# Performance work log

Measured on AMD Instinct MI355X. Metric: run time of the kernel, lower is better.

## Reference

```python
import jax, jax.numpy as jnp
import numpy as np

N = 200000   # nodes
E = 6400000  # edges (avg degree 32)
T = 6        # member feature dim
M = 10       # fingerprint dim
L = 4        # R + 1 layers
GIN = 14     # group_level_input
GLO = 10     # group_level_output


def setup_inputs() -> dict:
    key = jax.random.key(0)
    ks = jax.random.split(key, 10)
    return {
        "x_member": jax.random.normal(ks[0], (N, T), dtype=jnp.float32),
        "x_group": jax.random.normal(ks[1], (1, GIN), dtype=jnp.float32),
        "src": jax.random.randint(ks[2], (E,), 0, N, dtype=jnp.int32),
        "dst": jax.random.randint(ks[3], (E,), 0, N, dtype=jnp.int32),
        "H": jax.random.normal(ks[4], (L, T, M), dtype=jnp.float32),
        "W": jax.random.normal(ks[5], (L,), dtype=jnp.float32),
        "gW": jax.random.normal(ks[6], (GLO, GIN), dtype=jnp.float32) * 0.1,
        "gb": jax.random.normal(ks[7], (GLO,), dtype=jnp.float32),
        "mW": jax.random.normal(ks[8], (3, M + GLO), dtype=jnp.float32) * 0.1,
        "mb": jax.random.normal(ks[9], (3,), dtype=jnp.float32),
    }


def reference(x_member, x_group, src, dst, H, W, gW, gb, mW, mb):
    n = x_member.shape[0]
    # message passing: neighbor feature sum per destination node  [N, T]
    neigh = jax.ops.segment_sum(x_member[src], dst, num_segments=n)
    v1 = x_member + neigh  # r[a] + sum of neighbor r's; r is layer-invariant
    # all R+1 layers at once: [L, N, M]
    v2 = jax.nn.sigmoid(jnp.einsum("nt,ltm->lnm", v1, H))
    fl = jax.nn.softmax(v2 * W[:, None, None], axis=-1)
    # f starts at zeros and accumulates softmax over every node and layer -> [1, M]
    f = jnp.sum(fl, axis=(0, 1))[None, :]
    # group-level perceptron
    g = jax.nn.sigmoid(x_group @ gW.T + gb)  # [1, GLO]
    merged = jnp.concatenate([f, g], axis=1)  # [1, M+GLO]
    return jax.nn.softmax(merged @ mW.T + mb, axis=-1)  # [1, 3]
```

## Files before the change

### kernel.cpp

```cpp
#include <hip/hip_runtime.h>
#include <hip/hip_fp16.h>
#include <math.h>

#define TDIM 6
#define MDIM 10
#define LDIM 4
#define GIND 14
#define GLOD 10

#define BINSHIFT 8
#define BINSZ 256
#define MAXBINS 1024

#define SC2_BLOCKS 512
#define SC2_THREADS 512
#define SC2_KQ 7
#define OVF_ENT 16384
#define META2 2048

#define SC_BLOCK 512
#define SC_EPT 32
#define SC_EPB (SC_BLOCK * SC_EPT)
#define AC_BLOCK 512
#define AC_CAP 10240
#define AC_EPT 20

__global__ void zero32_k(unsigned* __restrict__ p, int n) {
    int i = blockIdx.x * blockDim.x + threadIdx.x;
    if (i < n) p[i] = 0u;
}


__global__ __launch_bounds__(SC2_THREADS) void scat2_k(
        const float* __restrict__ xm, int N, uint4* __restrict__ xh,
        const int* __restrict__ src, const int* __restrict__ dst, int E, int NQ, int QPB,
        unsigned* __restrict__ gcount, unsigned* __restrict__ ebuf, int C, int nbins,
        uint2* __restrict__ ovf, unsigned* __restrict__ ocur) {
    __shared__ unsigned lcount[MAXBINS];
    __shared__ unsigned lbase[MAXBINS];
    int tid = threadIdx.x;
    for (int i = tid; i < MAXBINS; i += SC2_THREADS) lcount[i] = 0u;

    int gid = blockIdx.x * SC2_THREADS + tid;
    int gstride = gridDim.x * SC2_THREADS;
    for (int n = gid; n < N; n += gstride) {
        const float2* r = (const float2*)(xm + (size_t)n * TDIM);
        float2 a = r[0], b = r[1], c = r[2];
        __half2 h0 = __floats2half2_rn(a.x, a.y);
        __half2 h1 = __floats2half2_rn(b.x, b.y);
        __half2 h2 = __floats2half2_rn(c.x, c.y);
        uint4 o;
        o.x = *(unsigned*)&h0; o.y = *(unsigned*)&h1; o.z = *(unsigned*)&h2; o.w = 0u;
        xh[n] = o;
    }
    if (blockIdx.x == 0) {
        for (int e = NQ * 4 + tid; e < E; e += SC2_THREADS) {
            unsigned oc = atomicAdd(ocur, 1u);
            if (oc < OVF_ENT) ovf[oc] = make_uint2((unsigned)src[e], (unsigned)dst[e]);
        }
    }
    __syncthreads();

    int qb = blockIdx.x * QPB;
    int qend = qb + QPB; if (qend > NQ) qend = NQ;
    const int4* s4p = (const int4*)src;
    const int4* d4p = (const int4*)dst;

    unsigned pk[SC2_KQ * 4];
    unsigned wr[SC2_KQ * 4];

#pragma unroll
    for (int i = 0; i < SC2_KQ; i++) {
        int q = qb + tid + i * SC2_THREADS;
        if (q < qend) {
            int4 sv = s4p[q];
            int4 dv = d4p[q];
            {
                unsigned du = (unsigned)dv.x, b = du >> BINSHIFT;
                pk[i*4+0] = ((du & (BINSZ-1)) << 18) | (unsigned)sv.x;
                wr[i*4+0] = (b << 18) | atomicAdd(&lcount[b], 1u);
            }
            {
                unsigned du = (unsigned)dv.y, b = du >> BINSHIFT;
                pk[i*4+1] = ((du & (BINSZ-1)) << 18) | (unsigned)sv.y;
                wr[i*4+1] = (b << 18) | atomicAdd(&lcount[b], 1u);
            }
            {
                unsigned du = (unsigned)dv.z, b = du >> BINSHIFT;
                pk[i*4+2] = ((du & (BINSZ-1)) << 18) | (unsigned)sv.z;
                wr[i*4+2] = (b << 18) | atomicAdd(&lcount[b], 1u);
            }
            {
                unsigned du = (unsigned)dv.w, b = du >> BINSHIFT;
                pk[i*4+3] = ((du & (BINSZ-1)) << 18) | (unsigned)sv.w;
                wr[i*4+3] = (b << 18) | atomicAdd(&lcount[b], 1u);
            }
        } else {
            pk[i*4+0] = 0xFFFFFFFFu; pk[i*4+1] = 0xFFFFFFFFu;
            pk[i*4+2] = 0xFFFFFFFFu; pk[i*4+3] = 0xFFFFFFFFu;
        }
    }
    __syncthreads();

    for (int i = tid; i < nbins; i += SC2_THREADS) {
        unsigned c = lcount[i];
        if (c) lbase[i] = atomicAdd(&gcount[i], c);
    }
    __syncthreads();

#pragma unroll
    for (int k = 0; k < SC2_KQ * 4; k++) {
        unsigned p = pk[k];
        if (p != 0xFFFFFFFFu) {
            unsigned b = wr[k] >> 18;
            unsigned pos = lbase[b] + (wr[k] & 0x3FFFFu);
            if (pos < (unsigned)C) {
                ebuf[b * (unsigned)C + pos] = p;
            } else {
                unsigned oc = atomicAdd(ocur, 1u);
                if (oc < OVF_ENT) {
                    unsigned s = p & 0x3FFFFu;
                    unsigned d = (b << BINSHIFT) | (p >> 18);
                    ovf[oc] = make_uint2(s, d);
                }
            }
        }
    }
}

__global__ __launch_bounds__(AC_BLOCK) void accum2_k(
        const float* __restrict__ xm, const uint4* __restrict__ xh,
        const unsigned* __restrict__ ebuf, const unsigned* __restrict__ gcount, int C,
        const unsigned* __restrict__ ocur, const uint2* __restrict__ ovf,
        const float* __restrict__ H, const float* __restrict__ W,
        float* __restrict__ facc, int N) {
    __shared__ unsigned srt[AC_CAP];
    __shared__ unsigned cnt[BINSZ];
    __shared__ unsigned tmp[BINSZ];
    __shared__ unsigned cstart[BINSZ];
    __shared__ unsigned ovl[256];
    __shared__ unsigned ovn;
    __shared__ float sH[LDIM * TDIM * MDIM];
    __shared__ float sW[LDIM];
    __shared__ float sred[AC_BLOCK / 64][MDIM];
    int tid = threadIdx.x;
    int bin = blockIdx.x;
    for (int i = tid; i < LDIM * TDIM * MDIM; i += AC_BLOCK) sH[i] = H[i];
    if (tid < LDIM) sW[tid] = W[tid];
    if (tid < BINSZ) cnt[tid] = 0u;
    if (tid == 0) ovn = 0u;
    __syncthreads();

    unsigned gc = gcount[bin];
    unsigned m = gc < (unsigned)C ? gc : (unsigned)C;
    unsigned e0 = (unsigned)bin * (unsigned)C;
    int nbase = bin << BINSHIFT;

    unsigned ed_[AC_EPT];
    unsigned rk_[AC_EPT];
#pragma unroll
    for (int k = 0; k < AC_EPT; k++) {
        unsigned i = (unsigned)tid + (unsigned)k * AC_BLOCK;
        if (i < m) {
            unsigned v = ebuf[e0 + i];
            ed_[k] = v;
            rk_[k] = atomicAdd(&cnt[v >> 18], 1u);
        }
    }
    {
        unsigned novf = *ocur;
        if (novf > OVF_ENT) novf = OVF_ENT;
        for (unsigned i = tid; i < novf; i += AC_BLOCK) {
            uint2 e = ovf[i];
            if ((e.y >> BINSHIFT) == (unsigned)bin) {
                unsigned u = atomicAdd(&ovn, 1u);
                if (u < 256u) ovl[u] = ((e.y & (BINSZ-1)) << 18) | e.x;
            }
        }
    }
    __syncthreads();

    if (tid < BINSZ) tmp[tid] = cnt[tid];
    __syncthreads();
    for (int off = 1; off < BINSZ; off <<= 1) {
        unsigned v = 0;
        if (tid < BINSZ) { v = tmp[tid]; if (tid >= off) v += tmp[tid - off]; }
        __syncthreads();
        if (tid < BINSZ) tmp[tid] = v;
        __syncthreads();
    }
    if (tid < BINSZ) cstart[tid] = tmp[tid] - cnt[tid];
    __syncthreads();

#pragma unroll
    for (int k = 0; k < AC_EPT; k++) {
        unsigned i = (unsigned)tid + (unsigned)k * AC_BLOCK;
        if (i < m) {
            unsigned v = ed_[k];
            srt[cstart[v >> 18] + rk_[k]] = v & 0x3FFFFu;
        }
    }
    __syncthreads();

    float fs[MDIM];
#pragma unroll
    for (int mm = 0; mm < MDIM; mm++) fs[mm] = 0.f;

    int n = nbase + tid;
    if (tid < BINSZ && n < N) {
        float s0 = 0.f, s1 = 0.f, s2 = 0.f, s3 = 0.f, s4 = 0.f, s5 = 0.f;
        unsigned c = cnt[tid];
        unsigned b0 = cstart[tid];
        unsigned j = 0;
        for (; j + 2 <= c; j += 2) {
            unsigned sa = srt[b0 + j], sb = srt[b0 + j + 1];
            uint4 ra = xh[sa];
            uint4 rb = xh[sb];
            float2 a0 = __half22float2(*(__half2*)&ra.x);
            float2 a1 = __half22float2(*(__half2*)&ra.y);
            float2 a2 = __half22float2(*(__half2*)&ra.z);
            float2 c0 = __half22float2(*(__half2*)&rb.x);
            float2 c1 = __half22float2(*(__half2*)&rb.y);
            float2 c2 = __half22float2(*(__half2*)&rb.z);
            s0 += a0.x + c0.x; s1 += a0.y + c0.y;
            s2 += a1.x + c1.x; s3 += a1.y + c1.y;
            s4 += a2.x + c2.x; s5 += a2.y + c2.y;
        }
        if (j < c) {
            uint4 ra = xh[srt[b0 + j]];
            float2 a0 = __half22float2(*(__half2*)&ra.x);
            float2 a1 = __half22float2(*(__half2*)&ra.y);
            float2 a2 = __half22float2(*(__half2*)&ra.z);
            s0 += a0.x; s1 += a0.y; s2 += a1.x; s3 += a1.y; s4 += a2.x; s5 += a2.y;
        }
        unsigned no = ovn < 256u ? ovn : 256u;
        for (unsigned q = 0; q < no; q++) {
            unsigned o = ovl[q];
            if ((int)(o >> 18) == tid) {
                uint4 ra = xh[o & 0x3FFFFu];
                float2 a0 = __half22float2(*(__half2*)&ra.x);
                float2 a1 = __half22float2(*(__half2*)&ra.y);
                float2 a2 = __half22float2(*(__half2*)&ra.z);
                s0 += a0.x; s1 += a0.y; s2 += a1.x; s3 += a1.y; s4 += a2.x; s5 += a2.y;
            }
        }

        float v[TDIM];
        const float2* xr = (const float2*)(xm + (size_t)n * TDIM);
        float2 x0 = xr[0], x1 = xr[1], x2 = xr[2];
        v[0] = x0.x + s0; v[1] = x0.y + s1;
        v[2] = x1.x + s2; v[3] = x1.y + s3;
        v[4] = x2.x + s4; v[5] = x2.y + s5;

#pragma unroll
        for (int l = 0; l < LDIM; l++) {
            float z[MDIM];
#pragma unroll
            for (int mm = 0; mm < MDIM; mm++) {
                float a2 = 0.f;
#pragma unroll
                for (int t = 0; t < TDIM; t++) a2 += v[t] * sH[(l * TDIM + t) * MDIM + mm];
                z[mm] = a2;
            }
            float wl = sW[l];
            float mx = -1e30f;
#pragma unroll
            for (int mm = 0; mm < MDIM; mm++) {
                float sg = wl / (1.f + __expf(-z[mm]));
                z[mm] = sg;
                mx = fmaxf(mx, sg);
            }
            float se = 0.f;
#pragma unroll
            for (int mm = 0; mm < MDIM; mm++) {
                float e = __expf(z[mm] - mx);
                z[mm] = e;
                se += e;
            }
            float inv = 1.f / se;
#pragma unroll
            for (int mm = 0; mm < MDIM; mm++) fs[mm] += z[mm] * inv;
        }
    }

#pragma unroll
    for (int mm = 0; mm < MDIM; mm++) {
        float v = fs[mm];
#pragma unroll
        for (int off = 32; off > 0; off >>= 1) v += __shfl_down(v, off, 64);
        fs[mm] = v;
    }
    int wave = tid >> 6, lane = tid & 63;
    if (lane == 0) {
#pragma unroll
        for (int mm = 0; mm < MDIM; mm++) sred[wave][mm] = fs[mm];
    }
    __syncthreads();
    if (tid < MDIM) {
        float s = 0.f;
#pragma unroll
        for (int w = 0; w < AC_BLOCK / 64; w++) s += sred[w][tid];
        atomicAdd(facc + tid, s);
    }
}


__global__ __launch_bounds__(256) void prep_k(const float* __restrict__ xm, int N,
                                              uint4* __restrict__ xh,
                                              const int* __restrict__ dst, int E,
                                              unsigned* __restrict__ hist, int nbins) {
    __shared__ unsigned lh[MAXBINS];
    for (int i = threadIdx.x; i < MAXBINS; i += blockDim.x) lh[i] = 0u;
    __syncthreads();
    int gid = blockIdx.x * blockDim.x + threadIdx.x;
    int gstride = gridDim.x * blockDim.x;
    for (int n = gid; n < N; n += gstride) {
        const float2* r = (const float2*)(xm + (size_t)n * TDIM);
        float2 a = r[0], b = r[1], c = r[2];
        __half2 h0 = __floats2half2_rn(a.x, a.y);
        __half2 h1 = __floats2half2_rn(b.x, b.y);
        __half2 h2 = __floats2half2_rn(c.x, c.y);
        uint4 o;
        o.x = *(unsigned*)&h0; o.y = *(unsigned*)&h1; o.z = *(unsigned*)&h2; o.w = 0u;
        xh[n] = o;
    }
    int e4 = E >> 2;
    const int4* d4p = (const int4*)dst;
    for (int i = gid; i < e4; i += gstride) {
        int4 d = d4p[i];
        atomicAdd(&lh[((unsigned)d.x) >> BINSHIFT], 1u);
        atomicAdd(&lh[((unsigned)d.y) >> BINSHIFT], 1u);
        atomicAdd(&lh[((unsigned)d.z) >> BINSHIFT], 1u);
        atomicAdd(&lh[((unsigned)d.w) >> BINSHIFT], 1u);
    }
    for (int e = (e4 << 2) + gid; e < E; e += gstride)
        atomicAdd(&lh[((unsigned)dst[e]) >> BINSHIFT], 1u);
    __syncthreads();
    for (int i = threadIdx.x; i < nbins; i += blockDim.x)
        if (lh[i]) atomicAdd(&hist[i], lh[i]);
}

__global__ __launch_bounds__(MAXBINS) void scan_k(const unsigned* __restrict__ hist,
                                                  unsigned* __restrict__ offsets,
                                                  unsigned* __restrict__ gfill, int nbins) {
    __shared__ unsigned buf[2][MAXBINS];
    int t = threadIdx.x;
    buf[0][t] = (t < nbins) ? hist[t] : 0u;
    __syncthreads();
    int cur = 0;
    for (int off = 1; off < MAXBINS; off <<= 1) {
        unsigned v = buf[cur][t];
        if (t >= off) v += buf[cur][t - off];
        buf[cur ^ 1][t] = v;
        __syncthreads();
        cur ^= 1;
    }
    if (t < nbins) {
        unsigned ex = t ? buf[cur][t - 1] : 0u;
        offsets[t] = ex;
        gfill[t] = ex;
    }
    if (t == 0) offsets[nbins] = buf[cur][nbins - 1];
}

__global__ __launch_bounds__(SC_BLOCK) void scatter_k(const int* __restrict__ src,
                                                      const int* __restrict__ dst, int E,
                                                      unsigned* __restrict__ gfill,
                                                      unsigned* __restrict__ ebuf, int nbins) {
    __shared__ unsigned lcount[MAXBINS];
    __shared__ unsigned lbase[MAXBINS];
    for (int i = threadIdx.x; i < MAXBINS; i += SC_BLOCK) lcount[i] = 0u;
    __syncthreads();
    int base = blockIdx.x * SC_EPB + threadIdx.x * SC_EPT;
    int s[SC_EPT], d[SC_EPT];
    unsigned rk[SC_EPT];
#pragma unroll
    for (int q = 0; q < SC_EPT / 4; q++) {
        int e = base + q * 4;
        if (e + 3 < E) {
            int4 s4 = *(const int4*)(src + e);
            int4 d4 = *(const int4*)(dst + e);
            s[q*4+0] = s4.x; s[q*4+1] = s4.y; s[q*4+2] = s4.z; s[q*4+3] = s4.w;
            d[q*4+0] = d4.x; d[q*4+1] = d4.y; d[q*4+2] = d4.z; d[q*4+3] = d4.w;
        } else {
#pragma unroll
            for (int k = 0; k < 4; k++) {
                int ee = e + k;
                s[q*4+k] = (ee < E) ? src[ee] : -1;
                d[q*4+k] = (ee < E) ? dst[ee] : 0;
            }
        }
    }
#pragma unroll
    for (int k = 0; k < SC_EPT; k++)
        if (s[k] >= 0) rk[k] = atomicAdd(&lcount[((unsigned)d[k]) >> BINSHIFT], 1u);
    __syncthreads();
    for (int i = threadIdx.x; i < nbins; i += SC_BLOCK) {
        unsigned c = lcount[i];
        if (c) lbase[i] = atomicAdd(&gfill[i], c);
    }
    __syncthreads();
#pragma unroll
    for (int k = 0; k < SC_EPT; k++) {
        if (s[k] >= 0) {
            unsigned du = (unsigned)d[k];
            unsigned b = du >> BINSHIFT;
            unsigned pack = ((du & (BINSZ - 1)) << 18) | (unsigned)s[k];
            ebuf[lbase[b] + rk[k]] = pack;
        }
    }
}

__global__ __launch_bounds__(AC_BLOCK) void accum_node_k(
        const float* __restrict__ xm, const uint4* __restrict__ xh,
        const unsigned* __restrict__ ebuf, const unsigned* __restrict__ offsets,
        const float* __restrict__ H, const float* __restrict__ W,
        float* __restrict__ facc, int N) {
    __shared__ unsigned srt[AC_CAP];
    __shared__ unsigned cnt[BINSZ];
    __shared__ unsigned tmp[BINSZ];
    __shared__ unsigned cstart[BINSZ];
    __shared__ float sH[LDIM * TDIM * MDIM];
    __shared__ float sW[LDIM];
    __shared__ float sred[AC_BLOCK / 64][MDIM];
    int tid = threadIdx.x;
    int bin = blockIdx.x;
    for (int i = tid; i < LDIM * TDIM * MDIM; i += AC_BLOCK) sH[i] = H[i];
    if (tid < LDIM) sW[tid] = W[tid];
    if (tid < BINSZ) cnt[tid] = 0u;
    __syncthreads();

    unsigned e0 = offsets[bin], e1 = offsets[bin + 1];
    unsigned total = e1 - e0;
    unsigned m = total < AC_CAP ? total : AC_CAP;
    int nbase = bin << BINSHIFT;

    unsigned ed_[AC_EPT];
    unsigned rk_[AC_EPT];
#pragma unroll
    for (int k = 0; k < AC_EPT; k++) {
        unsigned idx = e0 + (unsigned)tid + (unsigned)k * AC_BLOCK;
        if (idx < e0 + m) {
            unsigned v = ebuf[idx];
            ed_[k] = v;
            rk_[k] = atomicAdd(&cnt[v >> 18], 1u);
        }
    }
    __syncthreads();

    if (tid < BINSZ) tmp[tid] = cnt[tid];
    __syncthreads();
    for (int off = 1; off < BINSZ; off <<= 1) {
        unsigned v = 0;
        if (tid < BINSZ) { v = tmp[tid]; if (tid >= off) v += tmp[tid - off]; }
        __syncthreads();
        if (tid < BINSZ) tmp[tid] = v;
        __syncthreads();
    }
    if (tid < BINSZ) cstart[tid] = tmp[tid] - cnt[tid];
    __syncthreads();

#pragma unroll
    for (int k = 0; k < AC_EPT; k++) {
        unsigned idx = e0 + (unsigned)tid + (unsigned)k * AC_BLOCK;
        if (idx < e0 + m) {
            unsigned v = ed_[k];
            srt[cstart[v >> 18] + rk_[k]] = v & 0x3FFFFu;
        }
    }
    __syncthreads();

    float fs[MDIM];
#pragma unroll
    for (int mm = 0; mm < MDIM; mm++) fs[mm] = 0.f;

    int n = nbase + tid;
    if (tid < BINSZ && n < N) {
        float s0 = 0.f, s1 = 0.f, s2 = 0.f, s3 = 0.f, s4 = 0.f, s5 = 0.f;
        unsigned c = cnt[tid];
        unsigned b0 = cstart[tid];
        unsigned j = 0;
        for (; j + 2 <= c; j += 2) {
            unsigned sa = srt[b0 + j], sb = srt[b0 + j + 1];
            uint4 ra = xh[sa];
            uint4 rb = xh[sb];
            float2 a0 = __half22float2(*(__half2*)&ra.x);
            float2 a1 = __half22float2(*(__half2*)&ra.y);
            float2 a2 = __half22float2(*(__half2*)&ra.z);
            float2 c0 = __half22float2(*(__half2*)&rb.x);
            float2 c1 = __half22float2(*(__half2*)&rb.y);
            float2 c2 = __half22float2(*(__half2*)&rb.z);
            s0 += a0.x + c0.x; s1 += a0.y + c0.y;
            s2 += a1.x + c1.x; s3 += a1.y + c1.y;
            s4 += a2.x + c2.x; s5 += a2.y + c2.y;
        }
        if (j < c) {
            uint4 ra = xh[srt[b0 + j]];
            float2 a0 = __half22float2(*(__half2*)&ra.x);
            float2 a1 = __half22float2(*(__half2*)&ra.y);
            float2 a2 = __half22float2(*(__half2*)&ra.z);
            s0 += a0.x; s1 += a0.y; s2 += a1.x; s3 += a1.y; s4 += a2.x; s5 += a2.y;
        }
        for (unsigned idx = e0 + m; idx < e1; idx++) {
            unsigned v = ebuf[idx];
            if ((int)(v >> 18) == tid) {
                uint4 ra = xh[v & 0x3FFFFu];
                float2 a0 = __half22float2(*(__half2*)&ra.x);
                float2 a1 = __half22float2(*(__half2*)&ra.y);
                float2 a2 = __half22float2(*(__half2*)&ra.z);
                s0 += a0.x; s1 += a0.y; s2 += a1.x; s3 += a1.y; s4 += a2.x; s5 += a2.y;
            }
        }

        float v[TDIM];
        const float2* xr = (const float2*)(xm + (size_t)n * TDIM);
        float2 x0 = xr[0], x1 = xr[1], x2 = xr[2];
        v[0] = x0.x + s0; v[1] = x0.y + s1;
        v[2] = x1.x + s2; v[3] = x1.y + s3;
        v[4] = x2.x + s4; v[5] = x2.y + s5;

#pragma unroll
        for (int l = 0; l < LDIM; l++) {
            float z[MDIM];
#pragma unroll
            for (int mm = 0; mm < MDIM; mm++) {
                float a2 = 0.f;
#pragma unroll
                for (int t = 0; t < TDIM; t++) a2 += v[t] * sH[(l * TDIM + t) * MDIM + mm];
                z[mm] = a2;
            }
            float wl = sW[l];
            float mx = -1e30f;
#pragma unroll
            for (int mm = 0; mm < MDIM; mm++) {
                float sg = wl / (1.f + __expf(-z[mm]));
                z[mm] = sg;
                mx = fmaxf(mx, sg);
            }
            float se = 0.f;
#pragma unroll
            for (int mm = 0; mm < MDIM; mm++) {
                float e = __expf(z[mm] - mx);
                z[mm] = e;
                se += e;
            }
            float inv = 1.f / se;
#pragma unroll
            for (int mm = 0; mm < MDIM; mm++) fs[mm] += z[mm] * inv;
        }
    }

#pragma unroll
    for (int mm = 0; mm < MDIM; mm++) {
        float v = fs[mm];
#pragma unroll
        for (int off = 32; off > 0; off >>= 1) v += __shfl_down(v, off, 64);
        fs[mm] = v;
    }
    int wave = tid >> 6, lane = tid & 63;
    if (lane == 0) {
#pragma unroll
        for (int mm = 0; mm < MDIM; mm++) sred[wave][mm] = fs[mm];
    }
    __syncthreads();
    if (tid < MDIM) {
        float s = 0.f;
#pragma unroll
        for (int w = 0; w < AC_BLOCK / 64; w++) s += sred[w][tid];
        atomicAdd(facc + tid, s);
    }
}

__global__ void finalize_k(const float* __restrict__ facc,
                           const float* __restrict__ xg,
                           const float* __restrict__ gW,
                           const float* __restrict__ gb,
                           const float* __restrict__ mW,
                           const float* __restrict__ mb,
                           float* __restrict__ out) {
    if (threadIdx.x == 0 && blockIdx.x == 0) {
        float merged[MDIM + GLOD];
#pragma unroll
        for (int m = 0; m < MDIM; m++) merged[m] = facc[m];
        for (int j = 0; j < GLOD; j++) {
            float a = gb[j];
            for (int i = 0; i < GIND; i++) a += xg[i] * gW[j * GIND + i];
            merged[MDIM + j] = 1.f / (1.f + __expf(-a));
        }
        float lg[3];
        float mx = -1e30f;
        for (int k = 0; k < 3; k++) {
            float a = mb[k];
            for (int j = 0; j < MDIM + GLOD; j++) a += merged[j] * mW[k * (MDIM + GLOD) + j];
            lg[k] = a;
            mx = fmaxf(mx, a);
        }
        float se = 0.f;
        for (int k = 0; k < 3; k++) { lg[k] = __expf(lg[k] - mx); se += lg[k]; }
        float inv = 1.f / se;
        for (int k = 0; k < 3; k++) out[k] = lg[k] * inv;
    }
}

__global__ void fb_zero_k(float* __restrict__ ws, int n) {
    int i = blockIdx.x * blockDim.x + threadIdx.x;
    if (i < n) ws[i] = 0.f;
}

__global__ void fb_edge_scatter_k(const float* __restrict__ xm,
                                  const int* __restrict__ src,
                                  const int* __restrict__ dst,
                                  float* __restrict__ neigh, int E) {
    int e = blockIdx.x * blockDim.x + threadIdx.x;
    if (e >= E) return;
    int s = src[e], d = dst[e];
    const float2* r = (const float2*)(xm + (size_t)s * TDIM);
    float2 a = r[0], b = r[1], c = r[2];
    float* o = neigh + (size_t)d * TDIM;
    atomicAdd(o + 0, a.x); atomicAdd(o + 1, a.y);
    atomicAdd(o + 2, b.x); atomicAdd(o + 3, b.y);
    atomicAdd(o + 4, c.x); atomicAdd(o + 5, c.y);
}

__global__ __launch_bounds__(256) void fb_node_k(
        const float* __restrict__ xm, const float* __restrict__ neigh,
        const float* __restrict__ H, const float* __restrict__ W,
        float* __restrict__ facc, int N) {
    __shared__ float sH[LDIM * TDIM * MDIM];
    __shared__ float sW[LDIM];
    __shared__ float sred[4][MDIM];
    int tid = threadIdx.x;
    for (int i = tid; i < LDIM * TDIM * MDIM; i += blockDim.x) sH[i] = H[i];
    if (tid < LDIM) sW[tid] = W[tid];
    __syncthreads();
    float fs[MDIM];
#pragma unroll
    for (int m = 0; m < MDIM; m++) fs[m] = 0.f;
    for (int n = blockIdx.x * blockDim.x + tid; n < N; n += gridDim.x * blockDim.x) {
        float v[TDIM];
        const float2* xr = (const float2*)(xm + (size_t)n * TDIM);
        const float2* nr = (const float2*)(neigh + (size_t)n * TDIM);
#pragma unroll
        for (int t2 = 0; t2 < 3; t2++) {
            float2 a = xr[t2], b = nr[t2];
            v[2 * t2 + 0] = a.x + b.x;
            v[2 * t2 + 1] = a.y + b.y;
        }
#pragma unroll
        for (int l = 0; l < LDIM; l++) {
            float z[MDIM];
#pragma unroll
            for (int m = 0; m < MDIM; m++) {
                float a2 = 0.f;
#pragma unroll
                for (int t = 0; t < TDIM; t++) a2 += v[t] * sH[(l * TDIM + t) * MDIM + m];
                z[m] = a2;
            }
            float wl = sW[l], mx = -1e30f;
#pragma unroll
            for (int m = 0; m < MDIM; m++) { float sg = wl / (1.f + __expf(-z[m])); z[m] = sg; mx = fmaxf(mx, sg); }
            float se = 0.f;
#pragma unroll
            for (int m = 0; m < MDIM; m++) { float e = __expf(z[m] - mx); z[m] = e; se += e; }
            float inv = 1.f / se;
#pragma unroll
            for (int m = 0; m < MDIM; m++) fs[m] += z[m] * inv;
        }
    }
#pragma unroll
    for (int m = 0; m < MDIM; m++) {
        float v = fs[m];
#pragma unroll
        for (int off = 32; off > 0; off >>= 1) v += __shfl_down(v, off, 64);
        fs[m] = v;
    }
    int wave = tid >> 6, lane = tid & 63;
    if (lane == 0) {
#pragma unroll
        for (int m = 0; m < MDIM; m++) sred[wave][m] = fs[m];
    }
    __syncthreads();
    if (tid < MDIM) {
        float s = sred[0][tid] + sred[1][tid] + sred[2][tid] + sred[3][tid];
        atomicAdd(facc + tid, s);
    }
}

extern "C" void kernel_launch(void* const* d_in, const int* in_sizes, int n_in,
                              void* d_out, int out_size, void* d_ws, size_t ws_size,
                              hipStream_t stream) {
    const float* xm  = (const float*)d_in[0];
    const float* xg  = (const float*)d_in[1];
    const int*   src = (const int*)d_in[2];
    const int*   dst = (const int*)d_in[3];
    const float* H   = (const float*)d_in[4];
    const float* W   = (const float*)d_in[5];
    const float* gW  = (const float*)d_in[6];
    const float* gb  = (const float*)d_in[7];
    const float* mW  = (const float*)d_in[8];
    const float* mb  = (const float*)d_in[9];
    float* out = (float*)d_out;

    int N = in_sizes[0] / TDIM;
    int E = in_sizes[2];
    int nbins = (N + BINSZ - 1) >> BINSHIFT;
    size_t ws_words = ws_size / 4;
    size_t xh_words = (size_t)N * 4;

    long fixed = (long)(xh_words + META2 + (size_t)OVF_ENT * 2);
    long avail = (long)ws_words - fixed;
    long C = avail > 0 ? (avail / nbins) & ~3L : 0;
    if (C > AC_CAP) C = AC_CAP;
    double mu = (double)E / nbins;
    long Cmin = (long)(mu + 4.0 * sqrt(mu) + 32.0);
    int NQ = E >> 2;
    int QPB = (NQ + SC2_BLOCKS - 1) / SC2_BLOCKS;
    bool ok1 = (C >= Cmin) && nbins <= MAXBINS && N <= (1 << 18) &&
               QPB <= SC2_KQ * SC2_THREADS;

    size_t meta_words2 = MAXBINS + (MAXBINS + 1) + MAXBINS + 16;
    size_t need2 = (xh_words + (size_t)E + meta_words2) * 4;
    bool ok2 = ws_size >= need2 && nbins <= MAXBINS && N <= (1 << 18);

    if (ok1) {
        uint4*    xh     = (uint4*)d_ws;
        unsigned* ebuf   = (unsigned*)d_ws + xh_words;
        unsigned* gcount = ebuf + (size_t)nbins * C;
        unsigned* ocur   = gcount + MAXBINS;
        float*    facc   = (float*)(ocur + 16);
        uint2*    ovf    = (uint2*)(gcount + META2);

        zero32_k<<<(META2 + 255) / 256, 256, 0, stream>>>(gcount, META2);
        scat2_k<<<SC2_BLOCKS, SC2_THREADS, 0, stream>>>(xm, N, xh, src, dst, E, NQ, QPB,
                                                        gcount, ebuf, (int)C, nbins, ovf, ocur);
        accum2_k<<<nbins, AC_BLOCK, 0, stream>>>(xm, xh, ebuf, gcount, (int)C, ocur, ovf,
                                                 H, W, facc, N);
        finalize_k<<<1, 64, 0, stream>>>(facc, xg, gW, gb, mW, mb, out);
    } else if (ok2) {
        uint4*    xh      = (uint4*)d_ws;
        unsigned* ebuf    = (unsigned*)d_ws + xh_words;
        unsigned* hist    = ebuf + (size_t)E;
        unsigned* offsets = hist + MAXBINS;
        unsigned* gfill   = offsets + MAXBINS + 1;
        float*    facc    = (float*)(gfill + MAXBINS);

        zero32_k<<<(int)((meta_words2 + 255) / 256), 256, 0, stream>>>(hist, (int)meta_words2);
        prep_k<<<1024, 256, 0, stream>>>(xm, N, xh, dst, E, hist, nbins);
        scan_k<<<1, MAXBINS, 0, stream>>>(hist, offsets, gfill, nbins);
        scatter_k<<<(E + SC_EPB - 1) / SC_EPB, SC_BLOCK, 0, stream>>>(src, dst, E, gfill, ebuf, nbins);
        accum_node_k<<<nbins, AC_BLOCK, 0, stream>>>(xm, xh, ebuf, offsets, H, W, facc, N);
        finalize_k<<<1, 64, 0, stream>>>(facc, xg, gW, gb, mW, mb, out);
    } else {
        float* neigh = (float*)d_ws;
        float* facc  = neigh + (size_t)N * TDIM;
        int zn = N * TDIM + 16;
        fb_zero_k<<<(zn + 255) / 256, 256, 0, stream>>>(neigh, zn);
        fb_edge_scatter_k<<<(E + 255) / 256, 256, 0, stream>>>(xm, src, dst, neigh, E);
        fb_node_k<<<256, 256, 0, stream>>>(xm, neigh, H, W, facc, N);
        finalize_k<<<1, 64, 0, stream>>>(facc, xg, gW, gb, mW, mb, out);
    }
}
```

Baseline: 140.5 us.

## Split neighbor gather across both half-blocks and divide layers between them

In accum2_k the neighbor-row gather now uses all 512 threads. Each node's edge list is split into two halves handled by the two 256-thread halves, with partial sums combined through shared memory, and each half then evaluates two of the four layers. The gather loop is unrolled by four and uses nontemporal loads for the edge buffer and half-precision rows, and AC_CAP/AC_EPT shrink to cut register and LDS use. The aim is to remove the idle upper half-block and expose more memory-level parallelism, at the cost of an extra shared buffer and barrier, and more overflow edges now that AC_CAP is smaller.

```diff
diff --git a/kernel.cpp b/kernel.cpp
--- a/kernel.cpp
+++ b/kernel.cpp
@@ -22,8 +22,19 @@
 #define SC_EPT 32
 #define SC_EPB (SC_BLOCK * SC_EPT)
 #define AC_BLOCK 512
-#define AC_CAP 10240
-#define AC_EPT 20
+#define AC_CAP 8704
+#define AC_EPT 17
+
+typedef unsigned uvec4_t __attribute__((ext_vector_type(4)));
+
+__device__ __forceinline__ void add_row(uvec4_t r, float& s0, float& s1, float& s2,
+                                        float& s3, float& s4, float& s5) {
+    unsigned w0 = r[0], w1 = r[1], w2 = r[2];
+    float2 a0 = __half22float2(*(__half2*)&w0);
+    float2 a1 = __half22float2(*(__half2*)&w1);
+    float2 a2 = __half22float2(*(__half2*)&w2);
+    s0 += a0.x; s1 += a0.y; s2 += a1.x; s3 += a1.y; s4 += a2.x; s5 += a2.y;
+}
 
 __global__ void zero32_k(unsigned* __restrict__ p, int n) {
     int i = blockIdx.x * blockDim.x + threadIdx.x;
@@ -143,6 +154,7 @@
     __shared__ float sH[LDIM * TDIM * MDIM];
     __shared__ float sW[LDIM];
     __shared__ float sred[AC_BLOCK / 64][MDIM];
+    __shared__ float part[2][BINSZ][TDIM];
     int tid = threadIdx.x;
     int bin = blockIdx.x;
     for (int i = tid; i < LDIM * TDIM * MDIM; i += AC_BLOCK) sH[i] = H[i];
@@ -162,7 +174,7 @@
     for (int k = 0; k < AC_EPT; k++) {
         unsigned i = (unsigned)tid + (unsigned)k * AC_BLOCK;
         if (i < m) {
-            unsigned v = ebuf[e0 + i];
+            unsigned v = __builtin_nontemporal_load(ebuf + e0 + i);
             ed_[k] = v;
             rk_[k] = atomicAdd(&cnt[v >> 18], 1u);
         }
@@ -196,6 +208,287 @@
     for (int k = 0; k < AC_EPT; k++) {
         unsigned i = (unsigned)tid + (unsigned)k * AC_BLOCK;
         if (i < m) {
+            unsigned v = ed_[k];
+            srt[cstart[v >> 18] + rk_[k]] = v & 0x3FFFFu;
+        }
+    }
+    __syncthreads();
+
+    int node = tid & (BINSZ - 1);
+    int role = tid >> 8;
+    int n = nbase + node;
+    float s0 = 0.f, s1 = 0.f, s2 = 0.f, s3 = 0.f, s4 = 0.f, s5 = 0.f;
+    if (n < N) {
+        unsigned c = cnt[node];
+        unsigned b0 = cstart[node];
+        unsigned h = c >> 1;
+        unsigned j  = role ? h : 0u;
+        unsigned je = role ? c : h;
+        for (; j + 4 <= je; j += 4) {
+            unsigned ia = srt[b0 + j],     ib = srt[b0 + j + 1];
+            unsigned ic = srt[b0 + j + 2], id = srt[b0 + j + 3];
+            uvec4_t ra = __builtin_nontemporal_load((const uvec4_t*)(xh + ia));
+            uvec4_t rb = __builtin_nontemporal_load((const uvec4_t*)(xh + ib));
+            uvec4_t rc = __builtin_nontemporal_load((const uvec4_t*)(xh + ic));
+            uvec4_t rd = __builtin_nontemporal_load((const uvec4_t*)(xh + id));
+            add_row(ra, s0, s1, s2, s3, s4, s5);
+            add_row(rb, s0, s1, s2, s3, s4, s5);
+            add_row(rc, s0, s1, s2, s3, s4, s5);
+            add_row(rd, s0, s1, s2, s3, s4, s5);
+        }
+        for (; j < je; ++j) {
+            unsigned ia = srt[b0 + j];
+            uvec4_t ra = __builtin_nontemporal_load((const uvec4_t*)(xh + ia));
+            add_row(ra, s0, s1, s2, s3, s4, s5);
+        }
+        if (role == 0) {
+            unsigned no = ovn < 256u ? ovn : 256u;
+            for (unsigned q = 0; q < no; q++) {
+                unsigned o = ovl[q];
+                if ((int)(o >> 18) == node) {
+                    uint4 rr = xh[o & 0x3FFFFu];
+                    unsigned w0 = rr.x, w1 = rr.y, w2 = rr.z;
+                    float2 a0 = __half22float2(*(__half2*)&w0);
+                    float2 a1 = __half22float2(*(__half2*)&w1);
+                    float2 a2 = __half22float2(*(__half2*)&w2);
+                    s0 += a0.x; s1 += a0.y; s2 += a1.x; s3 += a1.y; s4 += a2.x; s5 += a2.y;
+                }
+            }
+        }
+    }
+    part[role][node][0] = s0; part[role][node][1] = s1; part[role][node][2] = s2;
+    part[role][node][3] = s3; part[role][node][4] = s4; part[role][node][5] = s5;
+    __syncthreads();
+
+    float fs[MDIM];
+#pragma unroll
+    for (int mm = 0; mm < MDIM; mm++) fs[mm] = 0.f;
+
+    if (n < N) {
+        float v[TDIM];
+        const float2* xr = (const float2*)(xm + (size_t)n * TDIM);
+        float2 x0 = xr[0], x1 = xr[1], x2 = xr[2];
+        v[0] = x0.x + part[0][node][0] + part[1][node][0];
+        v[1] = x0.y + part[0][node][1] + part[1][node][1];
+        v[2] = x1.x + part[0][node][2] + part[1][node][2];
+        v[3] = x1.y + part[0][node][3] + part[1][node][3];
+        v[4] = x2.x + part[0][node][4] + part[1][node][4];
+        v[5] = x2.y + part[0][node][5] + part[1][node][5];
+
+        int lb = role << 1;
+#pragma unroll
+        for (int li = 0; li < 2; li++) {
+            int l = lb + li;
+            float z[MDIM];
+#pragma unroll
+            for (int mm = 0; mm < MDIM; mm++) {
+                float a2 = 0.f;
+#pragma unroll
+                for (int t = 0; t < TDIM; t++) a2 += v[t] * sH[(l * TDIM + t) * MDIM + mm];
+                z[mm] = a2;
+            }
+            float wl = sW[l];
+            float mx = -1e30f;
+#pragma unroll
+            for (int mm = 0; mm < MDIM; mm++) {
+                float sg = wl / (1.f + __expf(-z[mm]));
+                z[mm] = sg;
+                mx = fmaxf(mx, sg);
+            }
+            float se = 0.f;
+#pragma unroll
+            for (int mm = 0; mm < MDIM; mm++) {
+                float e = __expf(z[mm] - mx);
+                z[mm] = e;
+                se += e;
+            }
+            float inv = 1.f / se;
+#pragma unroll
+            for (int mm = 0; mm < MDIM; mm++) fs[mm] += z[mm] * inv;
+        }
+    }
+
+#pragma unroll
+    for (int mm = 0; mm < MDIM; mm++) {
+        float v = fs[mm];
+#pragma unroll
+        for (int off = 32; off > 0; off >>= 1) v += __shfl_down(v, off, 64);
+        fs[mm] = v;
+    }
+    int wave = tid >> 6, lane = tid & 63;
+    if (lane == 0) {
+#pragma unroll
+        for (int mm = 0; mm < MDIM; mm++) sred[wave][mm] = fs[mm];
+    }
+    __syncthreads();
+    if (tid < MDIM) {
+        float s = 0.f;
+#pragma unroll
+        for (int w = 0; w < AC_BLOCK / 64; w++) s += sred[w][tid];
+        atomicAdd(facc + tid, s);
+    }
+}
+
+
+__global__ __launch_bounds__(256) void prep_k(const float* __restrict__ xm, int N,
+                                              uint4* __restrict__ xh,
+                                              const int* __restrict__ dst, int E,
+                                              unsigned* __restrict__ hist, int nbins) {
+    __shared__ unsigned lh[MAXBINS];
+    for (int i = threadIdx.x; i < MAXBINS; i += blockDim.x) lh[i] = 0u;
+    __syncthreads();
+    int gid = blockIdx.x * blockDim.x + threadIdx.x;
+    int gstride = gridDim.x * blockDim.x;
+    for (int n = gid; n < N; n += gstride) {
+        const float2* r = (const float2*)(xm + (size_t)n * TDIM);
+        float2 a = r[0], b = r[1], c = r[2];
+        __half2 h0 = __floats2half2_rn(a.x, a.y);
+        __half2 h1 = __floats2half2_rn(b.x, b.y);
+        __half2 h2 = __floats2half2_rn(c.x, c.y);
+        uint4 o;
+        o.x = *(unsigned*)&h0; o.y = *(unsigned*)&h1; o.z = *(unsigned*)&h2; o.w = 0u;
+        xh[n] = o;
+    }
+    int e4 = E >> 2;
+    const int4* d4p = (const int4*)dst;
+    for (int i = gid; i < e4; i += gstride) {
+        int4 d = d4p[i];
+        atomicAdd(&lh[((unsigned)d.x) >> BINSHIFT], 1u);
+        atomicAdd(&lh[((unsigned)d.y) >> BINSHIFT], 1u);
+        atomicAdd(&lh[((unsigned)d.z) >> BINSHIFT], 1u);
+        atomicAdd(&lh[((unsigned)d.w) >> BINSHIFT], 1u);
+    }
+    for (int e = (e4 << 2) + gid; e < E; e += gstride)
+        atomicAdd(&lh[((unsigned)dst[e]) >> BINSHIFT], 1u);
+    __syncthreads();
+    for (int i = threadIdx.x; i < nbins; i += blockDim.x)
+        if (lh[i]) atomicAdd(&hist[i], lh[i]);
+}
+
+__global__ __launch_bounds__(MAXBINS) void scan_k(const unsigned* __restrict__ hist,
+                                                  unsigned* __restrict__ offsets,
+                                                  unsigned* __restrict__ gfill, int nbins) {
+    __shared__ unsigned buf[2][MAXBINS];
+    int t = threadIdx.x;
+    buf[0][t] = (t < nbins) ? hist[t] : 0u;
+    __syncthreads();
+    int cur = 0;
+    for (int off = 1; off < MAXBINS; off <<= 1) {
+        unsigned v = buf[cur][t];
+        if (t >= off) v += buf[cur][t - off];
+        buf[cur ^ 1][t] = v;
+        __syncthreads();
+        cur ^= 1;
+    }
+    if (t < nbins) {
+        unsigned ex = t ? buf[cur][t - 1] : 0u;
+        offsets[t] = ex;
+        gfill[t] = ex;
+    }
+    if (t == 0) offsets[nbins] = buf[cur][nbins - 1];
+}
+
+__global__ __launch_bounds__(SC_BLOCK) void scatter_k(const int* __restrict__ src,
+                                                      const int* __restrict__ dst, int E,
+                                                      unsigned* __restrict__ gfill,
+                                                      unsigned* __restrict__ ebuf, int nbins) {
+    __shared__ unsigned lcount[MAXBINS];
+    __shared__ unsigned lbase[MAXBINS];
+    for (int i = threadIdx.x; i < MAXBINS; i += SC_BLOCK) lcount[i] = 0u;
+    __syncthreads();
+    int base = blockIdx.x * SC_EPB + threadIdx.x * SC_EPT;
+    int s[SC_EPT], d[SC_EPT];
+    unsigned rk[SC_EPT];
+#pragma unroll
+    for (int q = 0; q < SC_EPT / 4; q++) {
+        int e = base + q * 4;
+        if (e + 3 < E) {
+            int4 s4 = *(const int4*)(src + e);
+            int4 d4 = *(const int4*)(dst + e);
+            s[q*4+0] = s4.x; s[q*4+1] = s4.y; s[q*4+2] = s4.z; s[q*4+3] = s4.w;
+            d[q*4+0] = d4.x; d[q*4+1] = d4.y; d[q*4+2] = d4.z; d[q*4+3] = d4.w;
+        } else {
+#pragma unroll
+            for (int k = 0; k < 4; k++) {
+                int ee = e + k;
+                s[q*4+k] = (ee < E) ? src[ee] : -1;
+                d[q*4+k] = (ee < E) ? dst[ee] : 0;
+            }
+        }
+    }
+#pragma unroll
+    for (int k = 0; k < SC_EPT; k++)
+        if (s[k] >= 0) rk[k] = atomicAdd(&lcount[((unsigned)d[k]) >> BINSHIFT], 1u);
+    __syncthreads();
+    for (int i = threadIdx.x; i < nbins; i += SC_BLOCK) {
+        unsigned c = lcount[i];
+        if (c) lbase[i] = atomicAdd(&gfill[i], c);
+    }
+    __syncthreads();
+#pragma unroll
+    for (int k = 0; k < SC_EPT; k++) {
+        if (s[k] >= 0) {
+            unsigned du = (unsigned)d[k];
+            unsigned b = du >> BINSHIFT;
+            unsigned pack = ((du & (BINSZ - 1)) << 18) | (unsigned)s[k];
+            ebuf[lbase[b] + rk[k]] = pack;
+        }
+    }
+}
+
+__global__ __launch_bounds__(AC_BLOCK) void accum_node_k(
+        const float* __restrict__ xm, const uint4* __restrict__ xh,
+        const unsigned* __restrict__ ebuf, const unsigned* __restrict__ offsets,
+        const float* __restrict__ H, const float* __restrict__ W,
+        float* __restrict__ facc, int N) {
+    __shared__ unsigned srt[AC_CAP];
+    __shared__ unsigned cnt[BINSZ];
+    __shared__ unsigned tmp[BINSZ];
+    __shared__ unsigned cstart[BINSZ];
+    __shared__ float sH[LDIM * TDIM * MDIM];
+    __shared__ float sW[LDIM];
+    __shared__ float sred[AC_BLOCK / 64][MDIM];
+    int tid = threadIdx.x;
+    int bin = blockIdx.x;
+    for (int i = tid; i < LDIM * TDIM * MDIM; i += AC_BLOCK) sH[i] = H[i];
+    if (tid < LDIM) sW[tid] = W[tid];
+    if (tid < BINSZ) cnt[tid] = 0u;
+    __syncthreads();
+
+    unsigned e0 = offsets[bin], e1 = offsets[bin + 1];
+    unsigned total = e1 - e0;
+    unsigned m = total < AC_CAP ? total : AC_CAP;
+    int nbase = bin << BINSHIFT;
+
+    unsigned ed_[AC_EPT];
+    unsigned rk_[AC_EPT];
+#pragma unroll
+    for (int k = 0; k < AC_EPT; k++) {
+        unsigned idx = e0 + (unsigned)tid + (unsigned)k * AC_BLOCK;
+        if (idx < e0 + m) {
+            unsigned v = ebuf[idx];
+            ed_[k] = v;
+            rk_[k] = atomicAdd(&cnt[v >> 18], 1u);
+        }
+    }
+    __syncthreads();
+
+    if (tid < BINSZ) tmp[tid] = cnt[tid];
+    __syncthreads();
+    for (int off = 1; off < BINSZ; off <<= 1) {
+        unsigned v = 0;
+        if (tid < BINSZ) { v = tmp[tid]; if (tid >= off) v += tmp[tid - off]; }
+        __syncthreads();
+        if (tid < BINSZ) tmp[tid] = v;
+        __syncthreads();
+    }
+    if (tid < BINSZ) cstart[tid] = tmp[tid] - cnt[tid];
+    __syncthreads();
+
+#pragma unroll
+    for (int k = 0; k < AC_EPT; k++) {
+        unsigned idx = e0 + (unsigned)tid + (unsigned)k * AC_BLOCK;
+        if (idx < e0 + m) {
             unsigned v = ed_[k];
             srt[cstart[v >> 18] + rk_[k]] = v & 0x3FFFFu;
         }
@@ -233,274 +526,6 @@
             float2 a2 = __half22float2(*(__half2*)&ra.z);
             s0 += a0.x; s1 += a0.y; s2 += a1.x; s3 += a1.y; s4 += a2.x; s5 += a2.y;
         }
-        unsigned no = ovn < 256u ? ovn : 256u;
-        for (unsigned q = 0; q < no; q++) {
-            unsigned o = ovl[q];
-            if ((int)(o >> 18) == tid) {
-                uint4 ra = xh[o & 0x3FFFFu];
-                float2 a0 = __half22float2(*(__half2*)&ra.x);
-                float2 a1 = __half22float2(*(__half2*)&ra.y);
-                float2 a2 = __half22float2(*(__half2*)&ra.z);
-                s0 += a0.x; s1 += a0.y; s2 += a1.x; s3 += a1.y; s4 += a2.x; s5 += a2.y;
-            }
-        }
-
-        float v[TDIM];
-        const float2* xr = (const float2*)(xm + (size_t)n * TDIM);
-        float2 x0 = xr[0], x1 = xr[1], x2 = xr[2];
-        v[0] = x0.x + s0; v[1] = x0.y + s1;
-        v[2] = x1.x + s2; v[3] = x1.y + s3;
-        v[4] = x2.x + s4; v[5] = x2.y + s5;
-
-#pragma unroll
-        for (int l = 0; l < LDIM; l++) {
-            float z[MDIM];
-#pragma unroll
-            for (int mm = 0; mm < MDIM; mm++) {
-                float a2 = 0.f;
-#pragma unroll
-                for (int t = 0; t < TDIM; t++) a2 += v[t] * sH[(l * TDIM + t) * MDIM + mm];
-                z[mm] = a2;
-            }
-            float wl = sW[l];
-            float mx = -1e30f;
-#pragma unroll
-            for (int mm = 0; mm < MDIM; mm++) {
-                float sg = wl / (1.f + __expf(-z[mm]));
-                z[mm] = sg;
-                mx = fmaxf(mx, sg);
-            }
-            float se = 0.f;
-#pragma unroll
-            for (int mm = 0; mm < MDIM; mm++) {
-                float e = __expf(z[mm] - mx);
-                z[mm] = e;
-                se += e;
-            }
-            float inv = 1.f / se;
-#pragma unroll
-            for (int mm = 0; mm < MDIM; mm++) fs[mm] += z[mm] * inv;
-        }
-    }
-
-#pragma unroll
-    for (int mm = 0; mm < MDIM; mm++) {
-        float v = fs[mm];
-#pragma unroll
-        for (int off = 32; off > 0; off >>= 1) v += __shfl_down(v, off, 64);
-        fs[mm] = v;
-    }
-    int wave = tid >> 6, lane = tid & 63;
-    if (lane == 0) {
-#pragma unroll
-        for (int mm = 0; mm < MDIM; mm++) sred[wave][mm] = fs[mm];
-    }
-    __syncthreads();
-    if (tid < MDIM) {
-        float s = 0.f;
-#pragma unroll
-        for (int w = 0; w < AC_BLOCK / 64; w++) s += sred[w][tid];
-        atomicAdd(facc + tid, s);
-    }
-}
-
-
-__global__ __launch_bounds__(256) void prep_k(const float* __restrict__ xm, int N,
-                                              uint4* __restrict__ xh,
-                                              const int* __restrict__ dst, int E,
-                                              unsigned* __restrict__ hist, int nbins) {
-    __shared__ unsigned lh[MAXBINS];
-    for (int i = threadIdx.x; i < MAXBINS; i += blockDim.x) lh[i] = 0u;
-    __syncthreads();
-    int gid = blockIdx.x * blockDim.x + threadIdx.x;
-    int gstride = gridDim.x * blockDim.x;
-    for (int n = gid; n < N; n += gstride) {
-        const float2* r = (const float2*)(xm + (size_t)n * TDIM);
-        float2 a = r[0], b = r[1], c = r[2];
-        __half2 h0 = __floats2half2_rn(a.x, a.y);
-        __half2 h1 = __floats2half2_rn(b.x, b.y);
-        __half2 h2 = __floats2half2_rn(c.x, c.y);
-        uint4 o;
-        o.x = *(unsigned*)&h0; o.y = *(unsigned*)&h1; o.z = *(unsigned*)&h2; o.w = 0u;
-        xh[n] = o;
-    }
-    int e4 = E >> 2;
-    const int4* d4p = (const int4*)dst;
-    for (int i = gid; i < e4; i += gstride) {
-        int4 d = d4p[i];
-        atomicAdd(&lh[((unsigned)d.x) >> BINSHIFT], 1u);
-        atomicAdd(&lh[((unsigned)d.y) >> BINSHIFT], 1u);
-        atomicAdd(&lh[((unsigned)d.z) >> BINSHIFT], 1u);
-        atomicAdd(&lh[((unsigned)d.w) >> BINSHIFT], 1u);
-    }
-    for (int e = (e4 << 2) + gid; e < E; e += gstride)
-        atomicAdd(&lh[((unsigned)dst[e]) >> BINSHIFT], 1u);
-    __syncthreads();
-    for (int i = threadIdx.x; i < nbins; i += blockDim.x)
-        if (lh[i]) atomicAdd(&hist[i], lh[i]);
-}
-
-__global__ __launch_bounds__(MAXBINS) void scan_k(const unsigned* __restrict__ hist,
-                                                  unsigned* __restrict__ offsets,
-                                                  unsigned* __restrict__ gfill, int nbins) {
-    __shared__ unsigned buf[2][MAXBINS];
-    int t = threadIdx.x;
-    buf[0][t] = (t < nbins) ? hist[t] : 0u;
-    __syncthreads();
-    int cur = 0;
-    for (int off = 1; off < MAXBINS; off <<= 1) {
-        unsigned v = buf[cur][t];
-        if (t >= off) v += buf[cur][t - off];
-        buf[cur ^ 1][t] = v;
-        __syncthreads();
-        cur ^= 1;
-    }
-    if (t < nbins) {
-        unsigned ex = t ? buf[cur][t - 1] : 0u;
-        offsets[t] = ex;
-        gfill[t] = ex;
-    }
-    if (t == 0) offsets[nbins] = buf[cur][nbins - 1];
-}
-
-__global__ __launch_bounds__(SC_BLOCK) void scatter_k(const int* __restrict__ src,
-                                                      const int* __restrict__ dst, int E,
-                                                      unsigned* __restrict__ gfill,
-                                                      unsigned* __restrict__ ebuf, int nbins) {
-    __shared__ unsigned lcount[MAXBINS];
-    __shared__ unsigned lbase[MAXBINS];
-    for (int i = threadIdx.x; i < MAXBINS; i += SC_BLOCK) lcount[i] = 0u;
-    __syncthreads();
-    int base = blockIdx.x * SC_EPB + threadIdx.x * SC_EPT;
-    int s[SC_EPT], d[SC_EPT];
-    unsigned rk[SC_EPT];
-#pragma unroll
-    for (int q = 0; q < SC_EPT / 4; q++) {
-        int e = base + q * 4;
-        if (e + 3 < E) {
-            int4 s4 = *(const int4*)(src + e);
-            int4 d4 = *(const int4*)(dst + e);
-            s[q*4+0] = s4.x; s[q*4+1] = s4.y; s[q*4+2] = s4.z; s[q*4+3] = s4.w;
-            d[q*4+0] = d4.x; d[q*4+1] = d4.y; d[q*4+2] = d4.z; d[q*4+3] = d4.w;
-        } else {
-#pragma unroll
-            for (int k = 0; k < 4; k++) {
-                int ee = e + k;
-                s[q*4+k] = (ee < E) ? src[ee] : -1;
-                d[q*4+k] = (ee < E) ? dst[ee] : 0;
-            }
-        }
-    }
-#pragma unroll
-    for (int k = 0; k < SC_EPT; k++)
-        if (s[k] >= 0) rk[k] = atomicAdd(&lcount[((unsigned)d[k]) >> BINSHIFT], 1u);
-    __syncthreads();
-    for (int i = threadIdx.x; i < nbins; i += SC_BLOCK) {
-        unsigned c = lcount[i];
-        if (c) lbase[i] = atomicAdd(&gfill[i], c);
-    }
-    __syncthreads();
-#pragma unroll
-    for (int k = 0; k < SC_EPT; k++) {
-        if (s[k] >= 0) {
-            unsigned du = (unsigned)d[k];
-            unsigned b = du >> BINSHIFT;
-            unsigned pack = ((du & (BINSZ - 1)) << 18) | (unsigned)s[k];
-            ebuf[lbase[b] + rk[k]] = pack;
-        }
-    }
-}
-
-__global__ __launch_bounds__(AC_BLOCK) void accum_node_k(
-        const float* __restrict__ xm, const uint4* __restrict__ xh,
-        const unsigned* __restrict__ ebuf, const unsigned* __restrict__ offsets,
-        const float* __restrict__ H, const float* __restrict__ W,
-        float* __restrict__ facc, int N) {
-    __shared__ unsigned srt[AC_CAP];
-    __shared__ unsigned cnt[BINSZ];
-    __shared__ unsigned tmp[BINSZ];
-    __shared__ unsigned cstart[BINSZ];
-    __shared__ float sH[LDIM * TDIM * MDIM];
-    __shared__ float sW[LDIM];
-    __shared__ float sred[AC_BLOCK / 64][MDIM];
-    int tid = threadIdx.x;
-    int bin = blockIdx.x;
-    for (int i = tid; i < LDIM * TDIM * MDIM; i += AC_BLOCK) sH[i] = H[i];
-    if (tid < LDIM) sW[tid] = W[tid];
-    if (tid < BINSZ) cnt[tid] = 0u;
-    __syncthreads();
-
-    unsigned e0 = offsets[bin], e1 = offsets[bin + 1];
-    unsigned total = e1 - e0;
-    unsigned m = total < AC_CAP ? total : AC_CAP;
-    int nbase = bin << BINSHIFT;
-
-    unsigned ed_[AC_EPT];
-    unsigned rk_[AC_EPT];
-#pragma unroll
-    for (int k = 0; k < AC_EPT; k++) {
-        unsigned idx = e0 + (unsigned)tid + (unsigned)k * AC_BLOCK;
-        if (idx < e0 + m) {
-            unsigned v = ebuf[idx];
-            ed_[k] = v;
-            rk_[k] = atomicAdd(&cnt[v >> 18], 1u);
-        }
-    }
-    __syncthreads();
-
-    if (tid < BINSZ) tmp[tid] = cnt[tid];
-    __syncthreads();
-    for (int off = 1; off < BINSZ; off <<= 1) {
-        unsigned v = 0;
-        if (tid < BINSZ) { v = tmp[tid]; if (tid >= off) v += tmp[tid - off]; }
-        __syncthreads();
-        if (tid < BINSZ) tmp[tid] = v;
-        __syncthreads();
-    }
-    if (tid < BINSZ) cstart[tid] = tmp[tid] - cnt[tid];
-    __syncthreads();
-
-#pragma unroll
-    for (int k = 0; k < AC_EPT; k++) {
-        unsigned idx = e0 + (unsigned)tid + (unsigned)k * AC_BLOCK;
-        if (idx < e0 + m) {
-            unsigned v = ed_[k];
-            srt[cstart[v >> 18] + rk_[k]] = v & 0x3FFFFu;
-        }
-    }
-    __syncthreads();
-
-    float fs[MDIM];
-#pragma unroll
-    for (int mm = 0; mm < MDIM; mm++) fs[mm] = 0.f;
-
-    int n = nbase + tid;
-    if (tid < BINSZ && n < N) {
-        float s0 = 0.f, s1 = 0.f, s2 = 0.f, s3 = 0.f, s4 = 0.f, s5 = 0.f;
-        unsigned c = cnt[tid];
-        unsigned b0 = cstart[tid];
-        unsigned j = 0;
-        for (; j + 2 <= c; j += 2) {
-            unsigned sa = srt[b0 + j], sb = srt[b0 + j + 1];
-            uint4 ra = xh[sa];
-            uint4 rb = xh[sb];
-            float2 a0 = __half22float2(*(__half2*)&ra.x);
-            float2 a1 = __half22float2(*(__half2*)&ra.y);
-            float2 a2 = __half22float2(*(__half2*)&ra.z);
-            float2 c0 = __half22float2(*(__half2*)&rb.x);
-            float2 c1 = __half22float2(*(__half2*)&rb.y);
-            float2 c2 = __half22float2(*(__half2*)&rb.z);
-            s0 += a0.x + c0.x; s1 += a0.y + c0.y;
-            s2 += a1.x + c1.x; s3 += a1.y + c1.y;
-            s4 += a2.x + c2.x; s5 += a2.y + c2.y;
-        }
-        if (j < c) {
-            uint4 ra = xh[srt[b0 + j]];
-            float2 a0 = __half22float2(*(__half2*)&ra.x);
-            float2 a1 = __half22float2(*(__half2*)&ra.y);
-            float2 a2 = __half22float2(*(__half2*)&ra.z);
-            s0 += a0.x; s1 += a0.y; s2 += a1.x; s3 += a1.y; s4 += a2.x; s5 += a2.y;
-        }
         for (unsigned idx = e0 + m; idx < e1; idx++) {
             unsigned v = ebuf[idx];
             if ((int)(v >> 18) == tid) {
```

New measurement: 179.7 us. +28.0%, slower.
